# Kernel optimization log

Measured on AMD Instinct MI355X. Metric: run time of the kernel, lower is better.

The kernel has to match this reference:

```python
import jax, jax.numpy as jnp
import numpy as np

GRID = 112  # densepose predictor output resolution (hardcoded in forward)
D = 16      # CSE embedding dim (view(16, -1) in forward)


def setup_inputs() -> dict:
    key = jax.random.key(0)
    k1, k2 = jax.random.split(key)
    feats = jax.random.normal(k1, (2, D, GRID, GRID), dtype=jnp.float32)
    vertex_embeddings = jax.random.normal(k2, (27554, D), dtype=jnp.float32)
    return {"feats": feats, "vertex_embeddings": vertex_embeddings}


def reference(feats, vertex_embeddings):
    # feats: [B, 16, 112, 112]; vertex_embeddings: [M, 16]
    B = feats.shape[0]
    # per-pixel embeddings: [B, N, D] with N = 112*112 (matches feats[i].view(16,-1).T)
    x = feats.reshape(B, D, -1).transpose(0, 2, 1)
    x2 = jnp.sum(x * x, axis=-1, keepdims=True)            # [B, N, 1]
    v2 = jnp.sum(vertex_embeddings * vertex_embeddings, -1)  # [M]
    dist = x2 - 2.0 * jnp.einsum('bnd,md->bnm', x, vertex_embeddings) + v2
    dps = jnp.argmin(dist, axis=-1).reshape(B, GRID, GRID)  # [B, 112, 112] int
    return feats, dps
```

## Files before the change

kernel.cpp:

```cpp
#include <hip/hip_runtime.h>
#include <math.h>
#include <float.h>

#define GRIDP 112
#define NPIX (GRIDP * GRIDP)
#define D 16
#define TSA 3328
#define TSB 3072
#define G 4
#define TG 4
#define GRPB (TG * TSA)
#define NISS (GRPB / 1024)

typedef short s16x8 __attribute__((ext_vector_type(8)));
typedef float f32x16 __attribute__((ext_vector_type(16)));
typedef unsigned int uint32;
typedef const __attribute__((address_space(1))) uint32* gas_ptr;
typedef __attribute__((address_space(3))) uint32* las_ptr;

__device__ inline unsigned short f2bf(float x) {
    unsigned u = __float_as_uint(x);
    u += 0x7fffu + ((u >> 16) & 1u);
    return (unsigned short)(u >> 16);
}
__device__ inline float bf2f(unsigned short b) { return __uint_as_float(((unsigned)b) << 16); }

#define MFMA __builtin_amdgcn_mfma_f32_32x32x16_bf16

__device__ __forceinline__ void split_store_row(const float* x, char* base, int row) {
    unsigned short t0[D], t1[D], t2[D];
#pragma unroll
    for (int e = 0; e < D; ++e) {
        float v = x[e];
        unsigned short a = f2bf(v);  float r1 = v - bf2f(a);
        unsigned short b = f2bf(r1); float r2 = r1 - bf2f(b);
        t0[e] = a; t1[e] = b; t2[e] = f2bf(r2);
    }
#pragma unroll
    for (int h2 = 0; h2 < 2; ++h2) {
        char* p = base + h2 * 512 + row * 16;
        s16x8 v0, v1, v2s;
#pragma unroll
        for (int j = 0; j < 8; ++j) {
            v0[j] = (short)t0[h2 * 8 + j];
            v1[j] = (short)t1[h2 * 8 + j];
            v2s[j] = (short)t2[h2 * 8 + j];
        }
        *(s16x8*)(p)        = v0;
        *(s16x8*)(p + 1024) = v1;
        *(s16x8*)(p + 2048) = v2s;
    }
}

__global__ __launch_bounds__(256) void prep_fused(
    const float* __restrict__ verts, const float* __restrict__ feats,
    char* __restrict__ abuf, char* __restrict__ bbuf,
    float* __restrict__ v2p, float* __restrict__ outf,
    int M, int Mtiles, int NP, int PTiles, int nvb, int npb, int nf4)
{
    int bx = blockIdx.x;
    if (bx < nvb) {
        int mp = bx * 256 + threadIdx.x;
        if (mp >= Mtiles * 32) return;
        int tile = mp >> 5, row = mp & 31;
        float x[D]; float v2;
        if (mp < M) {
            const float4* r4 = (const float4*)(verts + (size_t)mp * D);
            float4 a = r4[0], b = r4[1], c = r4[2], d = r4[3];
            x[0]=a.x; x[1]=a.y; x[2]=a.z; x[3]=a.w;
            x[4]=b.x; x[5]=b.y; x[6]=b.z; x[7]=b.w;
            x[8]=c.x; x[9]=c.y; x[10]=c.z; x[11]=c.w;
            x[12]=d.x; x[13]=d.y; x[14]=d.z; x[15]=d.w;
            float s = 0.f;
#pragma unroll
            for (int e = 0; e < D; ++e) s = fmaf(x[e], x[e], s);
            v2 = s;
            v2p[mp] = s;
        } else {
#pragma unroll
            for (int e = 0; e < D; ++e) x[e] = 0.f;
            v2 = FLT_MAX;
        }
        size_t tb = (size_t)tile * TSA;
        int hv = (row >> 2) & 1, rv = (row & 3) + 4 * (row >> 3);
        *(float*)(abuf + tb + 3072 + hv * 64 + rv * 4) = v2;
        split_store_row(x, abuf + tb, row);
    } else if (bx < nvb + npb) {
        int p = (bx - nvb) * 256 + threadIdx.x;
        if (p >= PTiles * 32) return;
        int tile = p >> 5, colr = p & 31;
        float x[D];
        if (p < NP) {
            int b = p / NPIX, n = p - b * NPIX;
            const float* xf = feats + ((size_t)b * D) * NPIX + n;
#pragma unroll
            for (int e = 0; e < D; ++e) x[e] = -2.0f * xf[(size_t)e * NPIX];
        } else {
#pragma unroll
            for (int e = 0; e < D; ++e) x[e] = 0.f;
        }
        split_store_row(x, bbuf + (size_t)tile * TSB, colr);
    } else {
        int i = (bx - nvb - npb) * 256 + threadIdx.x;
        if (i < nf4)
            ((float4*)outf)[i] = ((const float4*)feats)[i];
    }
}

__device__ inline float mintree16(const f32x16& a) {
    float a0 = fminf(fminf(a[0],  a[1]),  a[2]);
    float a1 = fminf(fminf(a[3],  a[4]),  a[5]);
    float a2 = fminf(fminf(a[6],  a[7]),  a[8]);
    float a3 = fminf(fminf(a[9],  a[10]), a[11]);
    float a4 = fminf(fminf(a[12], a[13]), a[14]);
    float a5 = fminf(fminf(a0, a1), a[15]);
    float a6 = fminf(fminf(a2, a3), a4);
    return fminf(a5, a6);
}

__device__ __forceinline__ void stage_group(const char* gbase, char* lbase,
                                            int wid, int lane) {
    for (int i = wid; i < NISS; i += 4) {
        __builtin_amdgcn_global_load_lds(
            (gas_ptr)(gbase + i * 1024 + lane * 16),
            (las_ptr)(lbase + i * 1024),
            16, 0, 0);
    }
}

__global__ __launch_bounds__(256) void mfma_scan(
    const char* __restrict__ abuf, const char* __restrict__ bbuf,
    float* __restrict__ pval, int* __restrict__ ptile,
    int Mtiles, int chunk, int NP, int PTiles)
{
    __shared__ __align__(16) char smem[2][GRPB];
    int lane = threadIdx.x & 63;
    int wid  = threadIdx.x >> 6;
    int col  = lane & 31, h = lane >> 5;
    int ptb  = (blockIdx.x * 4 + wid) * G;

    s16x8 bh[G], bm[G], bl[G];
#pragma unroll
    for (int g = 0; g < G; ++g) {
        int pt = ptb + g;
        int ptc = pt < PTiles ? pt : PTiles - 1;
        const char* bb = bbuf + (size_t)ptc * TSB + (size_t)h * 512 + (size_t)col * 16;
        bh[g] = *(const s16x8*)bb;
        bm[g] = *(const s16x8*)(bb + 1024);
        bl[g] = *(const s16x8*)(bb + 2048);
    }

    int mt0 = blockIdx.y * chunk;
    int mt1 = mt0 + chunk; if (mt1 > Mtiles) mt1 = Mtiles;
    int nT   = mt1 - mt0;
    int nGrp = (nT + TG - 1) / TG;

    float best[G]; int btl[G];
#pragma unroll
    for (int g = 0; g < G; ++g) { best[g] = FLT_MAX; btl[g] = mt0; }

    const char* gsrc = abuf + (size_t)mt0 * TSA;

    stage_group(gsrc, smem[0], wid, lane);
    __syncthreads();

    int cur = 0;
    for (int grp = 0; grp < nGrp; ++grp) {
        if (grp + 1 < nGrp)
            stage_group(gsrc + (size_t)(grp + 1) * GRPB, smem[cur ^ 1], wid, lane);

        const char* lb = smem[cur];
        int tmax = nT - grp * TG; if (tmax > TG) tmax = TG;
        for (int t = 0; t < tmax; ++t) {
            const char* lt = lb + t * TSA;
            s16x8 ah = *(const s16x8*)(lt + (size_t)h * 512 + (size_t)col * 16);
            s16x8 am = *(const s16x8*)(lt + 1024 + (size_t)h * 512 + (size_t)col * 16);
            s16x8 al = *(const s16x8*)(lt + 2048 + (size_t)h * 512 + (size_t)col * 16);
            f32x16 c = *(const f32x16*)(lt + 3072 + (size_t)h * 64);

            f32x16 acc[G];
#pragma unroll
            for (int g = 0; g < G; ++g) acc[g] = MFMA(ah, bh[g], c, 0, 0, 0);
#pragma unroll
            for (int g = 0; g < G; ++g) acc[g] = MFMA(ah, bm[g], acc[g], 0, 0, 0);
#pragma unroll
            for (int g = 0; g < G; ++g) acc[g] = MFMA(am, bh[g], acc[g], 0, 0, 0);
#pragma unroll
            for (int g = 0; g < G; ++g) acc[g] = MFMA(ah, bl[g], acc[g], 0, 0, 0);
#pragma unroll
            for (int g = 0; g < G; ++g) acc[g] = MFMA(am, bm[g], acc[g], 0, 0, 0);
#pragma unroll
            for (int g = 0; g < G; ++g) acc[g] = MFMA(al, bh[g], acc[g], 0, 0, 0);

            int mt = mt0 + grp * TG + t;
#pragma unroll
            for (int g = 0; g < G; ++g) {
                float m = mintree16(acc[g]);
                if (m < best[g]) { btl[g] = mt; best[g] = m; }
            }
        }
        __syncthreads();
        cur ^= 1;
    }

#pragma unroll
    for (int g = 0; g < G; ++g) {
        float o = __shfl_xor(best[g], 32, 64);
        int  ot = __shfl_xor(btl[g], 32, 64);
        if (o < best[g] || (o == best[g] && ot < btl[g])) { best[g] = o; btl[g] = ot; }
    }
    if (lane < 32) {
        int s = blockIdx.y;
#pragma unroll
        for (int g = 0; g < G; ++g) {
            int pt = ptb + g;
            int px = pt * 32 + col;
            if (pt < PTiles && px < NP) {
                pval[(size_t)s * NP + px] = best[g];
                ptile[(size_t)s * NP + px] = btl[g];
            }
        }
    }
}

__global__ __launch_bounds__(256) void finalize(
    const float* __restrict__ pval, const int* __restrict__ ptile,
    const float* __restrict__ feats, const float* __restrict__ verts,
    const float* __restrict__ v2p, float* __restrict__ dps,
    int S, int NP, int M)
{
    int p = blockIdx.x * 256 + threadIdx.x;
    if (p >= NP) return;
    float bv = pval[p]; int bt = ptile[p];
    for (int s = 1; s < S; ++s) {
        float v = pval[(size_t)s * NP + p];
        int   t = ptile[(size_t)s * NP + p];
        if (v < bv || (v == bv && t < bt)) { bv = v; bt = t; }
    }
    int b = p / NPIX, n = p - b * NPIX;
    const float* xf = feats + ((size_t)b * D) * NPIX + n;
    float xs[D];
#pragma unroll
    for (int d2 = 0; d2 < D; ++d2) xs[d2] = -2.0f * xf[(size_t)d2 * NPIX];
    int m0 = bt * 32, m1 = m0 + 32; if (m1 > M) m1 = M;
    float best = FLT_MAX; int bi = m0;
    for (int m = m0; m < m1; ++m) {
        const float4* vr = (const float4*)(verts + (size_t)m * D);
        float4 a = vr[0], bq = vr[1], c = vr[2], d = vr[3];
        float acc = v2p[m];
        acc = fmaf(a.x, xs[0], acc);  acc = fmaf(a.y, xs[1], acc);
        acc = fmaf(a.z, xs[2], acc);  acc = fmaf(a.w, xs[3], acc);
        acc = fmaf(bq.x, xs[4], acc); acc = fmaf(bq.y, xs[5], acc);
        acc = fmaf(bq.z, xs[6], acc); acc = fmaf(bq.w, xs[7], acc);
        acc = fmaf(c.x, xs[8], acc);  acc = fmaf(c.y, xs[9], acc);
        acc = fmaf(c.z, xs[10], acc); acc = fmaf(c.w, xs[11], acc);
        acc = fmaf(d.x, xs[12], acc); acc = fmaf(d.y, xs[13], acc);
        acc = fmaf(d.z, xs[14], acc); acc = fmaf(d.w, xs[15], acc);
        if (acc < best) { best = acc; bi = m; }
    }
    dps[p] = (float)bi;
}

__global__ __launch_bounds__(256) void v2_kernel(const float* __restrict__ verts,
                                                 float* __restrict__ v2, int M) {
    int m = blockIdx.x * 256 + threadIdx.x;
    if (m >= M) return;
    const float4* r = (const float4*)(verts + (size_t)m * D);
    float4 a = r[0], b = r[1], c = r[2], d = r[3];
    v2[m] = ((a.x*a.x + a.y*a.y) + (a.z*a.z + a.w*a.w))
          + ((b.x*b.x + b.y*b.y) + (b.z*b.z + b.w*b.w))
          + ((c.x*c.x + c.y*c.y) + (c.z*c.z + c.w*c.w))
          + ((d.x*d.x + d.y*d.y) + (d.z*d.z + d.w*d.w));
}

__global__ __launch_bounds__(256) void argmin_partial(
    const float* __restrict__ feats, const float* __restrict__ verts,
    const float* __restrict__ v2, float* __restrict__ pval, int* __restrict__ pidx,
    int M, int NPtot, int chunk)
{
    int p = blockIdx.x * 256 + threadIdx.x;
    if (p >= NPtot) return;
    int b = p / NPIX, n = p - b * NPIX;
    const float* xf = feats + ((size_t)b * D) * NPIX + n;
    float x[D];
#pragma unroll
    for (int d2 = 0; d2 < D; ++d2) x[d2] = -2.0f * xf[(size_t)d2 * NPIX];
    int s = blockIdx.y;
    int m0 = s * chunk, m1 = m0 + chunk; if (m1 > M) m1 = M;
    float best = INFINITY; int bi = 0;
    for (int m = m0; m < m1; ++m) {
        const float* vr = verts + (size_t)m * D;
        float acc = v2[m];
#pragma unroll
        for (int d2 = 0; d2 < D; ++d2) acc = fmaf(vr[d2], x[d2], acc);
        if (acc < best) { best = acc; bi = m; }
    }
    pval[(size_t)s * NPtot + p] = best;
    pidx[(size_t)s * NPtot + p] = bi;
}

__global__ __launch_bounds__(256) void reduce_idx(
    const float* __restrict__ pval, const int* __restrict__ pidx,
    float* __restrict__ dps, int S, int NP)
{
    int p = blockIdx.x * 256 + threadIdx.x;
    if (p >= NP) return;
    float bv = pval[p]; int bi = pidx[p];
    for (int s = 1; s < S; ++s) {
        float v = pval[(size_t)s * NP + p];
        int   i = pidx[(size_t)s * NP + p];
        if (v < bv || (v == bv && i < bi)) { bv = v; bi = i; }
    }
    dps[p] = (float)bi;
}

extern "C" void kernel_launch(void* const* d_in, const int* in_sizes, int n_in,
                              void* d_out, int out_size, void* d_ws, size_t ws_size,
                              hipStream_t stream)
{
    const float* feats = (const float*)d_in[0];
    const float* verts = (const float*)d_in[1];
    int M          = in_sizes[1] / D;
    int feat_elems = in_sizes[0];
    int Bn         = feat_elems / (D * NPIX);
    int NP         = Bn * NPIX;
    float* out = (float*)d_out;

    int PTiles = (NP + 31) >> 5;
    int Mtiles = (M + 31) >> 5;

    size_t off = 0;
    auto alloc = [&](size_t sz) { size_t o = off; off = (off + sz + 255) & ~(size_t)255; return o; };
    size_t oBF = alloc((size_t)PTiles * TSB);
    size_t oAF = alloc((size_t)(Mtiles + 2 * TG) * TSA);
    size_t oV2 = alloc((size_t)M * 4);
    size_t base = off;

    int S = 32;
    while (S > 1 && base + (size_t)S * NP * 8 > ws_size) S >>= 1;

    if (base + (size_t)S * NP * 8 <= ws_size) {
        char*  bbuf = (char*)d_ws + oBF;
        char*  abuf = (char*)d_ws + oAF;
        float* v2p  = (float*)((char*)d_ws + oV2);
        float* pval = (float*)((char*)d_ws + base);
        int*   ptil = (int*)((char*)d_ws + base + (size_t)S * NP * 4);

        int nvb = (Mtiles * 32 + 255) / 256;
        int npb = (PTiles * 32 + 255) / 256;
        int nf4 = feat_elems / 4;
        int ncb = (nf4 + 255) / 256;
        prep_fused<<<dim3(nvb + npb + ncb), dim3(256), 0, stream>>>(
            verts, feats, abuf, bbuf, v2p, out, M, Mtiles, NP, PTiles, nvb, npb, nf4);

        int chunk = (Mtiles + S - 1) / S;
        mfma_scan<<<dim3((PTiles + 4 * G - 1) / (4 * G), S), dim3(256), 0, stream>>>(
            abuf, bbuf, pval, ptil, Mtiles, chunk, NP, PTiles);

        finalize<<<dim3((NP + 255) / 256), dim3(256), 0, stream>>>(
            pval, ptil, feats, verts, v2p, out + feat_elems, S, NP, M);
    } else {
        hipMemcpyAsync(out, feats, (size_t)feat_elems * sizeof(float),
                       hipMemcpyDeviceToDevice, stream);
        char* ws = (char*)d_ws;
        float* v2 = (float*)ws;
        size_t o2 = (((size_t)M * 4) + 255) & ~(size_t)255;
        int S2 = 16;
        while (S2 > 1 && o2 + (size_t)S2 * NP * 8 > ws_size) S2 >>= 1;
        float* pval = (float*)(ws + o2);
        int*   pidx = (int*)(ws + o2 + (size_t)S2 * NP * 4);
        int chunk = (M + S2 - 1) / S2;
        v2_kernel<<<dim3((M + 255) / 256), dim3(256), 0, stream>>>(verts, v2, M);
        argmin_partial<<<dim3((NP + 255) / 256, S2), dim3(256), 0, stream>>>(
            feats, verts, v2, pval, pidx, M, NP, chunk);
        reduce_idx<<<dim3((NP + 255) / 256), dim3(256), 0, stream>>>(
            pval, pidx, out + feat_elems, S2, NP);
    }
}
```

Before: 152.6 us.

## Reduce split-M partial argmins via packed 64-bit atomicMin and halve pixel tiles per wave

Partial (value, tile) results from each M-split are no longer written to S separate workspace slices. Instead, each pixel's float distance is mapped to an order-preserving unsigned value, packed with the tile index into a 64-bit key, and merged with atomicMin. Finalize then reads a single key per pixel, and the key buffer is initialised inside the prep kernel. Pixel tiles per wave drop from 4 to 2, which doubles the grid and cuts register pressure, and the full-group tile loop is unrolled. The cost is atomic contention across S=32 splits and each A tile being reused across fewer pixel tiles.

```diff
diff --git a/kernel.cpp b/kernel.cpp
--- a/kernel.cpp
+++ b/kernel.cpp
@@ -7,7 +7,7 @@
 #define D 16
 #define TSA 3328
 #define TSB 3072
-#define G 4
+#define G 2
 #define TG 4
 #define GRPB (TG * TSA)
 #define NISS (GRPB / 1024)
@@ -15,6 +15,7 @@
 typedef short s16x8 __attribute__((ext_vector_type(8)));
 typedef float f32x16 __attribute__((ext_vector_type(16)));
 typedef unsigned int uint32;
+typedef unsigned long long u64;
 typedef const __attribute__((address_space(1))) uint32* gas_ptr;
 typedef __attribute__((address_space(3))) uint32* las_ptr;
 
@@ -26,6 +27,11 @@
 __device__ inline float bf2f(unsigned short b) { return __uint_as_float(((unsigned)b) << 16); }
 
 #define MFMA __builtin_amdgcn_mfma_f32_32x32x16_bf16
+
+__device__ inline unsigned fmap(float f) {
+    unsigned b = __float_as_uint(f);
+    return (b & 0x80000000u) ? ~b : (b | 0x80000000u);
+}
 
 __device__ __forceinline__ void split_store_row(const float* x, char* base, int row) {
     unsigned short t0[D], t1[D], t2[D];
@@ -55,8 +61,8 @@
 __global__ __launch_bounds__(256) void prep_fused(
     const float* __restrict__ verts, const float* __restrict__ feats,
     char* __restrict__ abuf, char* __restrict__ bbuf,
-    float* __restrict__ v2p, float* __restrict__ outf,
-    int M, int Mtiles, int NP, int PTiles, int nvb, int npb, int nf4)
+    float* __restrict__ v2p, float* __restrict__ outf, u64* __restrict__ keys,
+    int M, int Mtiles, int NP, int PTiles, int nvb, int npb, int ncb, int nf4)
 {
     int bx = blockIdx.x;
     if (bx < nvb) {
@@ -100,10 +106,13 @@
             for (int e = 0; e < D; ++e) x[e] = 0.f;
         }
         split_store_row(x, bbuf + (size_t)tile * TSB, colr);
-    } else {
+    } else if (bx < nvb + npb + ncb) {
         int i = (bx - nvb - npb) * 256 + threadIdx.x;
         if (i < nf4)
             ((float4*)outf)[i] = ((const float4*)feats)[i];
+    } else {
+        int i = (bx - nvb - npb - ncb) * 256 + threadIdx.x;
+        if (i < NP) keys[i] = ~0ull;
     }
 }
 
@@ -128,10 +137,40 @@
     }
 }
 
+__device__ __forceinline__ void do_tile(
+    const char* lt, int h, int col,
+    const s16x8* bh, const s16x8* bm, const s16x8* bl,
+    int mt, float* best, int* btl)
+{
+    s16x8 ah = *(const s16x8*)(lt + (size_t)h * 512 + (size_t)col * 16);
+    s16x8 am = *(const s16x8*)(lt + 1024 + (size_t)h * 512 + (size_t)col * 16);
+    s16x8 al = *(const s16x8*)(lt + 2048 + (size_t)h * 512 + (size_t)col * 16);
+    f32x16 c = *(const f32x16*)(lt + 3072 + (size_t)h * 64);
+
+    f32x16 acc[G];
+#pragma unroll
+    for (int g = 0; g < G; ++g) acc[g] = MFMA(ah, bh[g], c, 0, 0, 0);
+#pragma unroll
+    for (int g = 0; g < G; ++g) acc[g] = MFMA(ah, bm[g], acc[g], 0, 0, 0);
+#pragma unroll
+    for (int g = 0; g < G; ++g) acc[g] = MFMA(am, bh[g], acc[g], 0, 0, 0);
+#pragma unroll
+    for (int g = 0; g < G; ++g) acc[g] = MFMA(ah, bl[g], acc[g], 0, 0, 0);
+#pragma unroll
+    for (int g = 0; g < G; ++g) acc[g] = MFMA(am, bm[g], acc[g], 0, 0, 0);
+#pragma unroll
+    for (int g = 0; g < G; ++g) acc[g] = MFMA(al, bh[g], acc[g], 0, 0, 0);
+
+#pragma unroll
+    for (int g = 0; g < G; ++g) {
+        float m = mintree16(acc[g]);
+        if (m < best[g]) { btl[g] = mt; best[g] = m; }
+    }
+}
+
 __global__ __launch_bounds__(256) void mfma_scan(
     const char* __restrict__ abuf, const char* __restrict__ bbuf,
-    float* __restrict__ pval, int* __restrict__ ptile,
-    int Mtiles, int chunk, int NP, int PTiles)
+    u64* __restrict__ keys, int Mtiles, int chunk, int NP, int PTiles)
 {
     __shared__ __align__(16) char smem[2][GRPB];
     int lane = threadIdx.x & 63;
@@ -170,34 +209,15 @@
             stage_group(gsrc + (size_t)(grp + 1) * GRPB, smem[cur ^ 1], wid, lane);
 
         const char* lb = smem[cur];
+        int mtb = mt0 + grp * TG;
         int tmax = nT - grp * TG; if (tmax > TG) tmax = TG;
-        for (int t = 0; t < tmax; ++t) {
-            const char* lt = lb + t * TSA;
-            s16x8 ah = *(const s16x8*)(lt + (size_t)h * 512 + (size_t)col * 16);
-            s16x8 am = *(const s16x8*)(lt + 1024 + (size_t)h * 512 + (size_t)col * 16);
-            s16x8 al = *(const s16x8*)(lt + 2048 + (size_t)h * 512 + (size_t)col * 16);
-            f32x16 c = *(const f32x16*)(lt + 3072 + (size_t)h * 64);
-
-            f32x16 acc[G];
-#pragma unroll
-            for (int g = 0; g < G; ++g) acc[g] = MFMA(ah, bh[g], c, 0, 0, 0);
-#pragma unroll
-            for (int g = 0; g < G; ++g) acc[g] = MFMA(ah, bm[g], acc[g], 0, 0, 0);
-#pragma unroll
-            for (int g = 0; g < G; ++g) acc[g] = MFMA(am, bh[g], acc[g], 0, 0, 0);
-#pragma unroll
-            for (int g = 0; g < G; ++g) acc[g] = MFMA(ah, bl[g], acc[g], 0, 0, 0);
-#pragma unroll
-            for (int g = 0; g < G; ++g) acc[g] = MFMA(am, bm[g], acc[g], 0, 0, 0);
-#pragma unroll
-            for (int g = 0; g < G; ++g) acc[g] = MFMA(al, bh[g], acc[g], 0, 0, 0);
-
-            int mt = mt0 + grp * TG + t;
-#pragma unroll
-            for (int g = 0; g < G; ++g) {
-                float m = mintree16(acc[g]);
-                if (m < best[g]) { btl[g] = mt; best[g] = m; }
-            }
+        if (tmax == TG) {
+#pragma unroll
+            for (int t = 0; t < TG; ++t)
+                do_tile(lb + t * TSA, h, col, bh, bm, bl, mtb + t, best, btl);
+        } else {
+            for (int t = 0; t < tmax; ++t)
+                do_tile(lb + t * TSA, h, col, bh, bm, bl, mtb + t, best, btl);
         }
         __syncthreads();
         cur ^= 1;
@@ -210,33 +230,27 @@
         if (o < best[g] || (o == best[g] && ot < btl[g])) { best[g] = o; btl[g] = ot; }
     }
     if (lane < 32) {
-        int s = blockIdx.y;
 #pragma unroll
         for (int g = 0; g < G; ++g) {
             int pt = ptb + g;
             int px = pt * 32 + col;
             if (pt < PTiles && px < NP) {
-                pval[(size_t)s * NP + px] = best[g];
-                ptile[(size_t)s * NP + px] = btl[g];
+                u64 key = ((u64)fmap(best[g]) << 32) | (unsigned)btl[g];
+                atomicMin(&keys[px], key);
             }
         }
     }
 }
 
 __global__ __launch_bounds__(256) void finalize(
-    const float* __restrict__ pval, const int* __restrict__ ptile,
+    const u64* __restrict__ keys,
     const float* __restrict__ feats, const float* __restrict__ verts,
     const float* __restrict__ v2p, float* __restrict__ dps,
-    int S, int NP, int M)
+    int NP, int M)
 {
     int p = blockIdx.x * 256 + threadIdx.x;
     if (p >= NP) return;
-    float bv = pval[p]; int bt = ptile[p];
-    for (int s = 1; s < S; ++s) {
-        float v = pval[(size_t)s * NP + p];
-        int   t = ptile[(size_t)s * NP + p];
-        if (v < bv || (v == bv && t < bt)) { bv = v; bt = t; }
-    }
+    int bt = (int)(unsigned)(keys[p] & 0xffffffffu);
     int b = p / NPIX, n = p - b * NPIX;
     const float* xf = feats + ((size_t)b * D) * NPIX + n;
     float xs[D];
@@ -334,31 +348,32 @@
     size_t oBF = alloc((size_t)PTiles * TSB);
     size_t oAF = alloc((size_t)(Mtiles + 2 * TG) * TSA);
     size_t oV2 = alloc((size_t)M * 4);
-    size_t base = off;
+    size_t oKY = alloc((size_t)NP * 8);
+    size_t need = off;
 
     int S = 32;
-    while (S > 1 && base + (size_t)S * NP * 8 > ws_size) S >>= 1;
-
-    if (base + (size_t)S * NP * 8 <= ws_size) {
+
+    if (need <= ws_size) {
         char*  bbuf = (char*)d_ws + oBF;
         char*  abuf = (char*)d_ws + oAF;
         float* v2p  = (float*)((char*)d_ws + oV2);
-        float* pval = (float*)((char*)d_ws + base);
-        int*   ptil = (int*)((char*)d_ws + base + (size_t)S * NP * 4);
+        u64*   keys = (u64*)((char*)d_ws + oKY);
 
         int nvb = (Mtiles * 32 + 255) / 256;
         int npb = (PTiles * 32 + 255) / 256;
         int nf4 = feat_elems / 4;
         int ncb = (nf4 + 255) / 256;
-        prep_fused<<<dim3(nvb + npb + ncb), dim3(256), 0, stream>>>(
-            verts, feats, abuf, bbuf, v2p, out, M, Mtiles, NP, PTiles, nvb, npb, nf4);
+        int nkb = (NP + 255) / 256;
+        prep_fused<<<dim3(nvb + npb + ncb + nkb), dim3(256), 0, stream>>>(
+            verts, feats, abuf, bbuf, v2p, out, keys,
+            M, Mtiles, NP, PTiles, nvb, npb, ncb, nf4);
 
         int chunk = (Mtiles + S - 1) / S;
         mfma_scan<<<dim3((PTiles + 4 * G - 1) / (4 * G), S), dim3(256), 0, stream>>>(
-            abuf, bbuf, pval, ptil, Mtiles, chunk, NP, PTiles);
+            abuf, bbuf, keys, Mtiles, chunk, NP, PTiles);
 
         finalize<<<dim3((NP + 255) / 256), dim3(256), 0, stream>>>(
-            pval, ptil, feats, verts, v2p, out + feat_elems, S, NP, M);
+            keys, feats, verts, v2p, out + feat_elems, NP, M);
     } else {
         hipMemcpyAsync(out, feats, (size_t)feat_elems * sizeof(float),
                        hipMemcpyDeviceToDevice, stream);
```

After: 145.0 us. 5.0% less time.
